# Optimization experiments

Measured on AMD Instinct MI355X. Metric: run time of the kernel, lower is better.

## Reference

```python
import jax, jax.numpy as jnp
import numpy as np


def setup_inputs() -> dict:
    key = jax.random.key(0)
    kq, kk, kv = jax.random.split(key, 3)
    B, H, S, D = 2, 16, 2048, 64
    Q = jax.random.normal(kq, (B, H, S, D), dtype=jnp.float32)
    K = jax.random.normal(kk, (B, H, S, D), dtype=jnp.float32)
    V = jax.random.normal(kv, (B, H, S, D), dtype=jnp.float32)
    # causal mask: 1 = keep, 0 = masked (masked_fill on mask == 0)
    mask = jnp.tril(jnp.ones((S, S), dtype=bool))[None, None, :, :]
    return {"V": V, "Q": Q, "K": K, "Fk": D, "mask": mask}


def reference(V, Q, K, Fk, mask):
    scale = 1.0 / jnp.sqrt(jnp.asarray(Fk, dtype=jnp.float32))
    # [B,H,S,S] scores
    C = jnp.einsum("bhqd,bhkd->bhqk", Q, K) * scale
    C = jnp.where(mask, C, jnp.asarray(-1e9, dtype=C.dtype))
    C = jax.nn.softmax(C, axis=-1)
    return jnp.einsum("bhqk,bhkd->bhqd", C, V)
```

## Files before the change

kernel.cpp:

```cpp
#include <hip/hip_runtime.h>
#include <hip/hip_bf16.h>

typedef __bf16 bf16x8 __attribute__((ext_vector_type(8)));
typedef __bf16 bf16x4 __attribute__((ext_vector_type(4)));
typedef __bf16 bf16x2 __attribute__((ext_vector_type(2)));
typedef float f32x4 __attribute__((ext_vector_type(4)));
typedef float f32x16 __attribute__((ext_vector_type(16)));

#define S_LEN 2048
#define D_DIM 64
#define NQT   32

static __device__ __forceinline__ unsigned pk2(float a, float b) {
  bf16x2 t; t[0] = (__bf16)a; t[1] = (__bf16)b;
  return __builtin_bit_cast(unsigned, t);
}

__global__ __launch_bounds__(256) void preprocess_kernel(
    const float* __restrict__ Kg, const float* __restrict__ Vg,
    unsigned char* __restrict__ Kb, unsigned char* __restrict__ Vt) {
  __shared__ float buf[2048];
  const int tid  = threadIdx.x;
  const int tile = blockIdx.x;
  const float* kg = Kg + (long)tile * 2048;
  const float* vg = Vg + (long)tile * 2048;
  unsigned char* kb = Kb + (long)tile * 4096;
  unsigned char* vt = Vt + (long)tile * 4096;

  const int l = tid & 63, f = tid >> 6, h = l >> 5;

  {
    const float* kr = kg + (l & 31) * 64 + f * 16 + h * 8;
    float4 a = *reinterpret_cast<const float4*>(kr);
    float4 b = *reinterpret_cast<const float4*>(kr + 4);
    bf16x8 t;
    t[0]=(__bf16)a.x; t[1]=(__bf16)a.y; t[2]=(__bf16)a.z; t[3]=(__bf16)a.w;
    t[4]=(__bf16)b.x; t[5]=(__bf16)b.y; t[6]=(__bf16)b.z; t[7]=(__bf16)b.w;
    *reinterpret_cast<bf16x8*>(kb + tid * 16) = t;
  }
  #pragma unroll
  for (int i = 0; i < 2; ++i) {
    int idx = tid + 256 * i;
    *reinterpret_cast<float4*>(buf + idx * 4) =
        *reinterpret_cast<const float4*>(vg + idx * 4);
  }
  __syncthreads();
  {
    int dt = f >> 1, ks = f & 1;
    int d  = dt * 32 + (l & 31);
    int k0 = ks * 16 + h * 8;
    bf16x8 t;
    #pragma unroll
    for (int j = 0; j < 8; ++j) t[j] = (__bf16)buf[(k0 + j) * 64 + d];
    *reinterpret_cast<bf16x8*>(vt + tid * 16) = t;
  }
}

__global__ __launch_bounds__(256, 4) void attn_fwd_pair(
    const float* __restrict__ Qg, const unsigned char* __restrict__ Kb,
    const unsigned char* __restrict__ Vt, float* __restrict__ Og) {
  __shared__ float o_sm[4][32][68];
  __shared__ float m_sm[4][32];
  __shared__ float l_sm[4][32];

  const int tid  = threadIdx.x;
  const int lane = tid & 63;
  const int w    = tid >> 6;
  const int qc   = lane & 31;
  const int h    = lane >> 5;

  const int lb = blockIdx.x;
  const int e  = lb & 7;
  const int s  = lb >> 3;
  const int bh = e + 8 * (s >> 5);
  const int pi = s & 31;
  const long base = (long)bh * (S_LEN * D_DIM);

  const unsigned char* kb_bh = Kb + (long)bh * 64 * 4096 + lane * 16;
  const unsigned char* vt_bh = Vt + (long)bh * 64 * 4096 + lane * 16;

  bf16x8 kfr[4], vfr[4];
  auto ldK = [&](int kt) {
    const unsigned char* p = kb_bh + (long)kt * 4096;
    #pragma unroll
    for (int t = 0; t < 4; ++t)
      kfr[t] = *reinterpret_cast<const bf16x8*>(p + t * 1024);
  };
  auto ldV = [&](int kt) {
    const unsigned char* p = vt_bh + (long)kt * 4096;
    #pragma unroll
    for (int t = 0; t < 4; ++t)
      vfr[t] = *reinterpret_cast<const bf16x8*>(p + t * 1024);
  };

  #pragma unroll
  for (int phase = 0; phase < 2; ++phase) {
    const int qg = phase ? pi : (63 - pi);
    const int q0 = qg * 32;
    const int NT = qg + 1;

    bf16x8 qf[4];
    {
      const float qsc = 0.125f * 1.44269504f;
      const float* qp = Qg + base + (long)(q0 + qc) * D_DIM + h * 8;
      #pragma unroll
      for (int t = 0; t < 4; ++t) {
        float4 f0 = *reinterpret_cast<const float4*>(qp + t * 16);
        float4 f1 = *reinterpret_cast<const float4*>(qp + t * 16 + 4);
        bf16x8 q;
        q[0]=(__bf16)(f0.x*qsc); q[1]=(__bf16)(f0.y*qsc);
        q[2]=(__bf16)(f0.z*qsc); q[3]=(__bf16)(f0.w*qsc);
        q[4]=(__bf16)(f1.x*qsc); q[5]=(__bf16)(f1.y*qsc);
        q[6]=(__bf16)(f1.z*qsc); q[7]=(__bf16)(f1.w*qsc);
        qf[t] = q;
      }
    }

    f32x16 po0, po1;
    #pragma unroll
    for (int r = 0; r < 16; ++r) { po0[r] = 0.f; po1[r] = 0.f; }
    float m_run = -1e30f, l_run = 0.f;

    ldK(w);
    ldV(w);

    for (int kt = w; kt < NT; kt += 4) {
      const bool more = (kt + 4 < NT);

      f32x16 sa;
      #pragma unroll
      for (int r = 0; r < 16; ++r) sa[r] = 0.f;
      __builtin_amdgcn_s_setprio(1);
      #pragma unroll
      for (int t = 0; t < 4; ++t)
        sa = __builtin_amdgcn_mfma_f32_32x32x16_bf16(kfr[t], qf[t], sa, 0, 0, 0);
      __builtin_amdgcn_s_setprio(0);

      if (more) ldK(kt + 4);

      if (kt == NT - 1) {
        #pragma unroll
        for (int r = 0; r < 16; ++r)
          if (((r & 3) + 8 * (r >> 2) + 4 * h) > qc) sa[r] = -1e30f;
      }

      float rmax;
      {
        float a0 = fmaxf(fmaxf(sa[0], sa[1]),  fmaxf(sa[2], sa[3]));
        float a1 = fmaxf(fmaxf(sa[4], sa[5]),  fmaxf(sa[6], sa[7]));
        float a2 = fmaxf(fmaxf(sa[8], sa[9]),  fmaxf(sa[10], sa[11]));
        float a3 = fmaxf(fmaxf(sa[12], sa[13]), fmaxf(sa[14], sa[15]));
        rmax = fmaxf(fmaxf(a0, a1), fmaxf(a2, a3));
        rmax = fmaxf(rmax, __shfl_xor(rmax, 32));
      }

      if (__any(rmax > m_run + 8.0f)) {
        float mn    = fmaxf(m_run, rmax);
        float alpha = exp2f(m_run - mn);
        m_run = mn;
        l_run *= alpha;
        #pragma unroll
        for (int r = 0; r < 16; ++r) {
          float ar = __shfl(alpha, (r & 3) + 8 * (r >> 2) + 4 * h);
          po0[r] *= ar;
          po1[r] *= ar;
        }
      }

      #pragma unroll
      for (int r = 0; r < 16; ++r) sa[r] = exp2f(sa[r] - m_run);
      {
        float s0 = (sa[0] + sa[1]) + (sa[2] + sa[3]);
        float s1 = (sa[4] + sa[5]) + (sa[6] + sa[7]);
        float s2 = (sa[8] + sa[9]) + (sa[10] + sa[11]);
        float s3 = (sa[12] + sa[13]) + (sa[14] + sa[15]);
        float rs = (s0 + s1) + (s2 + s3);
        l_run += rs + __shfl_xor(rs, 32);
      }

      bf16x8 pa0, pa1;
      {
        unsigned k0 = pk2(sa[0], sa[1]),   k1 = pk2(sa[2], sa[3]);
        unsigned k2 = pk2(sa[4], sa[5]),   k3 = pk2(sa[6], sa[7]);
        unsigned k4 = pk2(sa[8], sa[9]),   k5 = pk2(sa[10], sa[11]);
        unsigned k6 = pk2(sa[12], sa[13]), k7 = pk2(sa[14], sa[15]);
        unsigned x02 = h ? k0 : k2, x13 = h ? k1 : k3;
        unsigned x46 = h ? k4 : k6, x57 = h ? k5 : k7;
        unsigned p02 = (unsigned)__shfl_xor((int)x02, 32);
        unsigned p13 = (unsigned)__shfl_xor((int)x13, 32);
        unsigned p46 = (unsigned)__shfl_xor((int)x46, 32);
        unsigned p57 = (unsigned)__shfl_xor((int)x57, 32);
        union { unsigned u[4]; bf16x8 v; } a, b;
        a.u[0] = h ? p02 : k0;  a.u[1] = h ? p13 : k1;
        a.u[2] = h ? k2 : p02;  a.u[3] = h ? k3 : p13;
        b.u[0] = h ? p46 : k4;  b.u[1] = h ? p57 : k5;
        b.u[2] = h ? k6 : p46;  b.u[3] = h ? k7 : p57;
        pa0 = a.v;
        pa1 = b.v;
      }

      __builtin_amdgcn_s_setprio(1);
      po0 = __builtin_amdgcn_mfma_f32_32x32x16_bf16(pa0, vfr[0], po0, 0, 0, 0);
      po0 = __builtin_amdgcn_mfma_f32_32x32x16_bf16(pa1, vfr[1], po0, 0, 0, 0);
      po1 = __builtin_amdgcn_mfma_f32_32x32x16_bf16(pa0, vfr[2], po1, 0, 0, 0);
      po1 = __builtin_amdgcn_mfma_f32_32x32x16_bf16(pa1, vfr[3], po1, 0, 0, 0);
      __builtin_amdgcn_s_setprio(0);

      if (more) ldV(kt + 4);
    }

    if (phase) __syncthreads();
    #pragma unroll
    for (int r = 0; r < 16; ++r) {
      int crow = (r & 3) + 8 * (r >> 2) + 4 * h;
      o_sm[w][crow][qc]      = po0[r];
      o_sm[w][crow][qc + 32] = po1[r];
    }
    if (h == 0) { m_sm[w][qc] = m_run; l_sm[w][qc] = l_run; }
    __syncthreads();

    {
      const int q  = tid >> 3;
      const int d0 = (tid & 7) * 8;
      float m0 = m_sm[0][q], m1 = m_sm[1][q];
      float m2 = m_sm[2][q], m3 = m_sm[3][q];
      float M  = fmaxf(fmaxf(m0, m1), fmaxf(m2, m3));
      float a0 = exp2f(m0 - M), a1 = exp2f(m1 - M);
      float a2 = exp2f(m2 - M), a3 = exp2f(m3 - M);
      float inv = 1.0f / (a0 * l_sm[0][q] + a1 * l_sm[1][q]
                        + a2 * l_sm[2][q] + a3 * l_sm[3][q]);
      float* og = Og + base + (long)(q0 + q) * D_DIM + d0;
      #pragma unroll
      for (int half = 0; half < 2; ++half) {
        float4 x0 = *reinterpret_cast<const float4*>(&o_sm[0][q][d0 + 4 * half]);
        float4 x1 = *reinterpret_cast<const float4*>(&o_sm[1][q][d0 + 4 * half]);
        float4 x2 = *reinterpret_cast<const float4*>(&o_sm[2][q][d0 + 4 * half]);
        float4 x3 = *reinterpret_cast<const float4*>(&o_sm[3][q][d0 + 4 * half]);
        float4 o;
        o.x = (a0 * x0.x + a1 * x1.x + a2 * x2.x + a3 * x3.x) * inv;
        o.y = (a0 * x0.y + a1 * x1.y + a2 * x2.y + a3 * x3.y) * inv;
        o.z = (a0 * x0.z + a1 * x1.z + a2 * x2.z + a3 * x3.z) * inv;
        o.w = (a0 * x0.w + a1 * x1.w + a2 * x2.w + a3 * x3.w) * inv;
        *reinterpret_cast<float4*>(og + 4 * half) = o;
      }
    }
  }
}

__global__ __launch_bounds__(256) void attn_fwd_fallback(
    const float* __restrict__ Vg, const float* __restrict__ Qg,
    const float* __restrict__ Kg, float* __restrict__ Og) {
  __shared__ __align__(16) unsigned char k_lds[64 * 128];
  __shared__ __align__(16) unsigned char vt_lds[64 * 128];
  __shared__ __align__(16) unsigned char p_lds[4][16 * 128];

  const int tid  = threadIdx.x;
  const int lane = tid & 63;
  const int w    = tid >> 6;
  const int lr   = lane & 15;
  const int lg   = lane >> 4;
  const int swz  = (lr & 7) << 4;

  const int lb = blockIdx.x;
  const int e  = lb & 7;
  const int s  = lb >> 3;
  const int bh = e + 8 * (s >> 5);
  const int qs = s & 31;
  const int qt = (qs & 1) ? (NQT - 1 - (qs >> 1)) : (qs >> 1);
  const long base = (long)bh * (S_LEN * D_DIM);
  const int q0 = qt * 64;

  bf16x8 qf[2];
  {
    const float qsc = 0.125f * 1.44269504f;
    const float* qp = Qg + base + (q0 + w * 16 + lr) * D_DIM + lg * 8;
    #pragma unroll
    for (int c = 0; c < 2; ++c) {
      float4 f0 = *reinterpret_cast<const float4*>(qp + c * 32);
      float4 f1 = *reinterpret_cast<const float4*>(qp + c * 32 + 4);
      bf16x8 t;
      t[0]=(__bf16)(f0.x*qsc); t[1]=(__bf16)(f0.y*qsc);
      t[2]=(__bf16)(f0.z*qsc); t[3]=(__bf16)(f0.w*qsc);
      t[4]=(__bf16)(f1.x*qsc); t[5]=(__bf16)(f1.y*qsc);
      t[6]=(__bf16)(f1.z*qsc); t[7]=(__bf16)(f1.w*qsc);
      qf[c] = t;
    }
  }
  bf16x8 onesf;
  #pragma unroll
  for (int j = 0; j < 8; ++j) onesf[j] = (lr == 0) ? (__bf16)1.0f : (__bf16)0.0f;

  f32x4 po[4], pl;
  float m_run = -1e30f;
  #pragma unroll
  for (int j = 0; j < 4; ++j) po[j] = (f32x4){0.f,0.f,0.f,0.f};
  pl = (f32x4){0.f,0.f,0.f,0.f};

  float4 kreg[4];
  float  vreg[16];
  const int d_ = lane;
  const int kb = w;

  auto load_regs = [&](int kt) {
    const float* kg = Kg + base + kt * (64 * D_DIM);
    #pragma unroll
    for (int i = 0; i < 4; ++i) {
      int idx = tid + 256 * i;
      int r = idx >> 4, f4 = idx & 15;
      kreg[i] = *reinterpret_cast<const float4*>(kg + r * 64 + f4 * 4);
    }
    const float* vg = Vg + base + kt * (64 * D_DIM);
    #pragma unroll
    for (int j = 0; j < 8; ++j) {
      vreg[j]     = vg[(kb * 8 + j) * 64 + d_];
      vreg[8 + j] = vg[((kb + 4) * 8 + j) * 64 + d_];
    }
  };
  auto write_buf = [&]() {
    #pragma unroll
    for (int i = 0; i < 4; ++i) {
      int idx = tid + 256 * i;
      int r = idx >> 4, f4 = idx & 15;
      bf16x4 t;
      t[0]=(__bf16)kreg[i].x; t[1]=(__bf16)kreg[i].y;
      t[2]=(__bf16)kreg[i].z; t[3]=(__bf16)kreg[i].w;
      int b = r * 128 + ((f4 * 8) ^ ((r & 7) << 4));
      *reinterpret_cast<bf16x4*>(&k_lds[b]) = t;
    }
    bf16x8 t0, t1;
    #pragma unroll
    for (int j = 0; j < 8; ++j) { t0[j] = (__bf16)vreg[j]; t1[j] = (__bf16)vreg[8+j]; }
    int b0 = d_ * 128 + ((kb * 16) ^ ((d_ & 7) << 4));
    int b1 = d_ * 128 + (((kb + 4) * 16) ^ ((d_ & 7) << 4));
    *reinterpret_cast<bf16x8*>(&vt_lds[b0]) = t0;
    *reinterpret_cast<bf16x8*>(&vt_lds[b1]) = t1;
  };

  load_regs(0);
  write_buf();
  __syncthreads();

  for (int kt = 0; kt <= qt; ++kt) {
    const bool last = (kt == qt);
    if (!last) load_regs(kt + 1);

    f32x4 sa[4];
    #pragma unroll
    for (int ct = 0; ct < 4; ++ct) sa[ct] = (f32x4){0.f,0.f,0.f,0.f};
    #pragma unroll
    for (int ct = 0; ct < 4; ++ct) {
      #pragma unroll
      for (int c = 0; c < 2; ++c) {
        int b = (ct * 16 + lr) * 128 + ((lg * 16 + c * 64) ^ swz);
        bf16x8 kf = *reinterpret_cast<const bf16x8*>(&k_lds[b]);
        sa[ct] = __builtin_amdgcn_mfma_f32_16x16x32_bf16(kf, qf[c], sa[ct], 0, 0, 0);
      }
    }
    if (last) {
      #pragma unroll
      for (int ct = 0; ct < 4; ++ct)
        #pragma unroll
        for (int j = 0; j < 4; ++j)
          if (ct * 16 + lg * 4 + j > w * 16 + lr) sa[ct][j] = -1e30f;
    }
    float rmax = sa[0][0];
    #pragma unroll
    for (int ct = 0; ct < 4; ++ct)
      #pragma unroll
      for (int j = 0; j < 4; ++j) rmax = fmaxf(rmax, sa[ct][j]);
    rmax = fmaxf(rmax, __shfl_xor(rmax, 16));
    rmax = fmaxf(rmax, __shfl_xor(rmax, 32));
    float mn    = fmaxf(m_run, rmax);
    float alpha = exp2f(m_run - mn);
    m_run = mn;
    #pragma unroll
    for (int ct = 0; ct < 4; ++ct) {
      bf16x4 t;
      #pragma unroll
      for (int j = 0; j < 4; ++j) t[j] = (__bf16)exp2f(sa[ct][j] - mn);
      int b = lr * 128 + ((ct * 32 + lg * 8) ^ swz);
      *reinterpret_cast<bf16x4*>(&p_lds[w][b]) = t;
    }
    float aj[4];
    #pragma unroll
    for (int j = 0; j < 4; ++j) aj[j] = __shfl(alpha, (lane & 48) | (lg * 4 + j));
    #pragma unroll
    for (int j = 0; j < 4; ++j) {
      pl[j] *= aj[j];
      #pragma unroll
      for (int dt = 0; dt < 4; ++dt) po[dt][j] *= aj[j];
    }
    #pragma unroll
    for (int c = 0; c < 2; ++c) {
      int ab = lr * 128 + ((lg * 16 + c * 64) ^ swz);
      bf16x8 pa = *reinterpret_cast<const bf16x8*>(&p_lds[w][ab]);
      pl = __builtin_amdgcn_mfma_f32_16x16x32_bf16(pa, onesf, pl, 0, 0, 0);
      #pragma unroll
      for (int dt = 0; dt < 4; ++dt) {
        int vb_ = (dt * 16 + lr) * 128 + ((lg * 16 + c * 64) ^ swz);
        bf16x8 vb = *reinterpret_cast<const bf16x8*>(&vt_lds[vb_]);
        po[dt] = __builtin_amdgcn_mfma_f32_16x16x32_bf16(pa, vb, po[dt], 0, 0, 0);
      }
    }
    if (!last) {
      __syncthreads();
      write_buf();
      __syncthreads();
    }
  }
  #pragma unroll
  for (int j = 0; j < 4; ++j) {
    float lv  = __shfl(pl[j], lane & 48);
    float inv = 1.0f / lv;
    int row = q0 + w * 16 + lg * 4 + j;
    #pragma unroll
    for (int dt = 0; dt < 4; ++dt)
      Og[base + row * D_DIM + dt * 16 + lr] = po[dt][j] * inv;
  }
}

extern "C" void kernel_launch(void* const* d_in, const int* in_sizes, int n_in,
                              void* d_out, int out_size, void* d_ws, size_t ws_size,
                              hipStream_t stream) {
  const float* V = (const float*)d_in[0];
  const float* Q = (const float*)d_in[1];
  const float* K = (const float*)d_in[2];
  float* O = (float*)d_out;
  const size_t need = (size_t)2 * 32 * 64 * 4096;
  if (ws_size >= need) {
    unsigned char* Kb = (unsigned char*)d_ws;
    unsigned char* Vt = Kb + (size_t)32 * 64 * 4096;
    preprocess_kernel<<<dim3(2048), dim3(256), 0, stream>>>(K, V, Kb, Vt);
    attn_fwd_pair<<<dim3(1024), dim3(256), 0, stream>>>(Q, Kb, Vt, O);
  } else {
    attn_fwd_fallback<<<dim3(1024), dim3(256), 0, stream>>>(V, Q, K, O);
  }
}
```

Baseline: 61.91 us.

## Process two 32-row query tiles per workgroup to reuse K/V fragments

Each workgroup now handles a 64-row query block as two 32-row sub-tiles that share every loaded K and V fragment, halving K/V global traffic per query. The grid shrinks from 1024 to 512 blocks and the launch bound drops to 2 waves per SIMD to make room for the doubled accumulators. The causal diagonal is handled by skipping sub-tile A on the last key tile and masking each sub-tile on its own diagonal tile. The risks are lower occupancy, less latency hiding, and fewer blocks to balance the causal work across CUs.

```diff
diff --git a/kernel.cpp b/kernel.cpp
--- a/kernel.cpp
+++ b/kernel.cpp
@@ -56,7 +56,7 @@
   }
 }
 
-__global__ __launch_bounds__(256, 4) void attn_fwd_pair(
+__global__ __launch_bounds__(256, 2) void attn_fwd_q64(
     const float* __restrict__ Qg, const unsigned char* __restrict__ Kb,
     const unsigned char* __restrict__ Vt, float* __restrict__ Og) {
   __shared__ float o_sm[4][32][68];
@@ -69,11 +69,11 @@
   const int qc   = lane & 31;
   const int h    = lane >> 5;
 
-  const int lb = blockIdx.x;
-  const int e  = lb & 7;
-  const int s  = lb >> 3;
-  const int bh = e + 8 * (s >> 5);
-  const int pi = s & 31;
+  const int b  = blockIdx.x;
+  const int e  = b & 7;
+  const int s  = b >> 3;
+  const int bh = e + 8 * (s >> 4);
+  const int pi = s & 15;
   const long base = (long)bh * (S_LEN * D_DIM);
 
   const unsigned char* kb_bh = Kb + (long)bh * 64 * 4096 + lane * 16;
@@ -93,123 +93,69 @@
       vfr[t] = *reinterpret_cast<const bf16x8*>(p + t * 1024);
   };
 
-  #pragma unroll
-  for (int phase = 0; phase < 2; ++phase) {
-    const int qg = phase ? pi : (63 - pi);
-    const int q0 = qg * 32;
-    const int NT = qg + 1;
-
-    bf16x8 qf[4];
+  auto process = [&](f32x16& sa, float& m_run, float& l_run,
+                     f32x16& po0, f32x16& po1) {
+    float rmax;
     {
-      const float qsc = 0.125f * 1.44269504f;
-      const float* qp = Qg + base + (long)(q0 + qc) * D_DIM + h * 8;
-      #pragma unroll
-      for (int t = 0; t < 4; ++t) {
-        float4 f0 = *reinterpret_cast<const float4*>(qp + t * 16);
-        float4 f1 = *reinterpret_cast<const float4*>(qp + t * 16 + 4);
-        bf16x8 q;
-        q[0]=(__bf16)(f0.x*qsc); q[1]=(__bf16)(f0.y*qsc);
-        q[2]=(__bf16)(f0.z*qsc); q[3]=(__bf16)(f0.w*qsc);
-        q[4]=(__bf16)(f1.x*qsc); q[5]=(__bf16)(f1.y*qsc);
-        q[6]=(__bf16)(f1.z*qsc); q[7]=(__bf16)(f1.w*qsc);
-        qf[t] = q;
-      }
-    }
-
-    f32x16 po0, po1;
-    #pragma unroll
-    for (int r = 0; r < 16; ++r) { po0[r] = 0.f; po1[r] = 0.f; }
-    float m_run = -1e30f, l_run = 0.f;
-
-    ldK(w);
-    ldV(w);
-
-    for (int kt = w; kt < NT; kt += 4) {
-      const bool more = (kt + 4 < NT);
-
-      f32x16 sa;
-      #pragma unroll
-      for (int r = 0; r < 16; ++r) sa[r] = 0.f;
-      __builtin_amdgcn_s_setprio(1);
-      #pragma unroll
-      for (int t = 0; t < 4; ++t)
-        sa = __builtin_amdgcn_mfma_f32_32x32x16_bf16(kfr[t], qf[t], sa, 0, 0, 0);
-      __builtin_amdgcn_s_setprio(0);
-
-      if (more) ldK(kt + 4);
-
-      if (kt == NT - 1) {
-        #pragma unroll
-        for (int r = 0; r < 16; ++r)
-          if (((r & 3) + 8 * (r >> 2) + 4 * h) > qc) sa[r] = -1e30f;
-      }
-
-      float rmax;
-      {
-        float a0 = fmaxf(fmaxf(sa[0], sa[1]),  fmaxf(sa[2], sa[3]));
-        float a1 = fmaxf(fmaxf(sa[4], sa[5]),  fmaxf(sa[6], sa[7]));
-        float a2 = fmaxf(fmaxf(sa[8], sa[9]),  fmaxf(sa[10], sa[11]));
-        float a3 = fmaxf(fmaxf(sa[12], sa[13]), fmaxf(sa[14], sa[15]));
-        rmax = fmaxf(fmaxf(a0, a1), fmaxf(a2, a3));
-        rmax = fmaxf(rmax, __shfl_xor(rmax, 32));
-      }
-
-      if (__any(rmax > m_run + 8.0f)) {
-        float mn    = fmaxf(m_run, rmax);
-        float alpha = exp2f(m_run - mn);
-        m_run = mn;
-        l_run *= alpha;
-        #pragma unroll
-        for (int r = 0; r < 16; ++r) {
-          float ar = __shfl(alpha, (r & 3) + 8 * (r >> 2) + 4 * h);
-          po0[r] *= ar;
-          po1[r] *= ar;
-        }
-      }
-
-      #pragma unroll
-      for (int r = 0; r < 16; ++r) sa[r] = exp2f(sa[r] - m_run);
-      {
-        float s0 = (sa[0] + sa[1]) + (sa[2] + sa[3]);
-        float s1 = (sa[4] + sa[5]) + (sa[6] + sa[7]);
-        float s2 = (sa[8] + sa[9]) + (sa[10] + sa[11]);
-        float s3 = (sa[12] + sa[13]) + (sa[14] + sa[15]);
-        float rs = (s0 + s1) + (s2 + s3);
-        l_run += rs + __shfl_xor(rs, 32);
-      }
-
-      bf16x8 pa0, pa1;
-      {
-        unsigned k0 = pk2(sa[0], sa[1]),   k1 = pk2(sa[2], sa[3]);
-        unsigned k2 = pk2(sa[4], sa[5]),   k3 = pk2(sa[6], sa[7]);
-        unsigned k4 = pk2(sa[8], sa[9]),   k5 = pk2(sa[10], sa[11]);
-        unsigned k6 = pk2(sa[12], sa[13]), k7 = pk2(sa[14], sa[15]);
-        unsigned x02 = h ? k0 : k2, x13 = h ? k1 : k3;
-        unsigned x46 = h ? k4 : k6, x57 = h ? k5 : k7;
-        unsigned p02 = (unsigned)__shfl_xor((int)x02, 32);
-        unsigned p13 = (unsigned)__shfl_xor((int)x13, 32);
-        unsigned p46 = (unsigned)__shfl_xor((int)x46, 32);
-        unsigned p57 = (unsigned)__shfl_xor((int)x57, 32);
-        union { unsigned u[4]; bf16x8 v; } a, b;
-        a.u[0] = h ? p02 : k0;  a.u[1] = h ? p13 : k1;
-        a.u[2] = h ? k2 : p02;  a.u[3] = h ? k3 : p13;
-        b.u[0] = h ? p46 : k4;  b.u[1] = h ? p57 : k5;
-        b.u[2] = h ? k6 : p46;  b.u[3] = h ? k7 : p57;
-        pa0 = a.v;
-        pa1 = b.v;
-      }
-
-      __builtin_amdgcn_s_setprio(1);
-      po0 = __builtin_amdgcn_mfma_f32_32x32x16_bf16(pa0, vfr[0], po0, 0, 0, 0);
-      po0 = __builtin_amdgcn_mfma_f32_32x32x16_bf16(pa1, vfr[1], po0, 0, 0, 0);
-      po1 = __builtin_amdgcn_mfma_f32_32x32x16_bf16(pa0, vfr[2], po1, 0, 0, 0);
-      po1 = __builtin_amdgcn_mfma_f32_32x32x16_bf16(pa1, vfr[3], po1, 0, 0, 0);
-      __builtin_amdgcn_s_setprio(0);
-
-      if (more) ldV(kt + 4);
-    }
-
-    if (phase) __syncthreads();
+      float a0 = fmaxf(fmaxf(sa[0], sa[1]),  fmaxf(sa[2], sa[3]));
+      float a1 = fmaxf(fmaxf(sa[4], sa[5]),  fmaxf(sa[6], sa[7]));
+      float a2 = fmaxf(fmaxf(sa[8], sa[9]),  fmaxf(sa[10], sa[11]));
+      float a3 = fmaxf(fmaxf(sa[12], sa[13]), fmaxf(sa[14], sa[15]));
+      rmax = fmaxf(fmaxf(a0, a1), fmaxf(a2, a3));
+      rmax = fmaxf(rmax, __shfl_xor(rmax, 32));
+    }
+    if (__any(rmax > m_run + 8.0f)) {
+      float mn    = fmaxf(m_run, rmax);
+      float alpha = exp2f(m_run - mn);
+      m_run = mn;
+      l_run *= alpha;
+      #pragma unroll
+      for (int r = 0; r < 16; ++r) {
+        float ar = __shfl(alpha, (r & 3) + 8 * (r >> 2) + 4 * h);
+        po0[r] *= ar;
+        po1[r] *= ar;
+      }
+    }
+    #pragma unroll
+    for (int r = 0; r < 16; ++r) sa[r] = exp2f(sa[r] - m_run);
+    {
+      float s0 = (sa[0] + sa[1]) + (sa[2] + sa[3]);
+      float s1 = (sa[4] + sa[5]) + (sa[6] + sa[7]);
+      float s2 = (sa[8] + sa[9]) + (sa[10] + sa[11]);
+      float s3 = (sa[12] + sa[13]) + (sa[14] + sa[15]);
+      float rs = (s0 + s1) + (s2 + s3);
+      l_run += rs + __shfl_xor(rs, 32);
+    }
+    bf16x8 pa0, pa1;
+    {
+      unsigned k0 = pk2(sa[0], sa[1]),   k1 = pk2(sa[2], sa[3]);
+      unsigned k2 = pk2(sa[4], sa[5]),   k3 = pk2(sa[6], sa[7]);
+      unsigned k4 = pk2(sa[8], sa[9]),   k5 = pk2(sa[10], sa[11]);
+      unsigned k6 = pk2(sa[12], sa[13]), k7 = pk2(sa[14], sa[15]);
+      unsigned x02 = h ? k0 : k2, x13 = h ? k1 : k3;
+      unsigned x46 = h ? k4 : k6, x57 = h ? k5 : k7;
+      unsigned p02 = (unsigned)__shfl_xor((int)x02, 32);
+      unsigned p13 = (unsigned)__shfl_xor((int)x13, 32);
+      unsigned p46 = (unsigned)__shfl_xor((int)x46, 32);
+      unsigned p57 = (unsigned)__shfl_xor((int)x57, 32);
+      union { unsigned u[4]; bf16x8 v; } a2, b2;
+      a2.u[0] = h ? p02 : k0;  a2.u[1] = h ? p13 : k1;
+      a2.u[2] = h ? k2 : p02;  a2.u[3] = h ? k3 : p13;
+      b2.u[0] = h ? p46 : k4;  b2.u[1] = h ? p57 : k5;
+      b2.u[2] = h ? k6 : p46;  b2.u[3] = h ? k7 : p57;
+      pa0 = a2.v;
+      pa1 = b2.v;
+    }
+    __builtin_amdgcn_s_setprio(1);
+    po0 = __builtin_amdgcn_mfma_f32_32x32x16_bf16(pa0, vfr[0], po0, 0, 0, 0);
+    po0 = __builtin_amdgcn_mfma_f32_32x32x16_bf16(pa1, vfr[1], po0, 0, 0, 0);
+    po1 = __builtin_amdgcn_mfma_f32_32x32x16_bf16(pa0, vfr[2], po1, 0, 0, 0);
+    po1 = __builtin_amdgcn_mfma_f32_32x32x16_bf16(pa1, vfr[3], po1, 0, 0, 0);
+    __builtin_amdgcn_s_setprio(0);
+  };
+
+  auto submerge = [&](const f32x16& po0, const f32x16& po1,
+                      float m_run, float l_run, int qbase) {
     #pragma unroll
     for (int r = 0; r < 16; ++r) {
       int crow = (r & 3) + 8 * (r >> 2) + 4 * h;
@@ -218,7 +164,6 @@
     }
     if (h == 0) { m_sm[w][qc] = m_run; l_sm[w][qc] = l_run; }
     __syncthreads();
-
     {
       const int q  = tid >> 3;
       const int d0 = (tid & 7) * 8;
@@ -229,7 +174,7 @@
       float a2 = exp2f(m2 - M), a3 = exp2f(m3 - M);
       float inv = 1.0f / (a0 * l_sm[0][q] + a1 * l_sm[1][q]
                         + a2 * l_sm[2][q] + a3 * l_sm[3][q]);
-      float* og = Og + base + (long)(q0 + q) * D_DIM + d0;
+      float* og = Og + base + (long)(qbase + q) * D_DIM + d0;
       #pragma unroll
       for (int half = 0; half < 2; ++half) {
         float4 x0 = *reinterpret_cast<const float4*>(&o_sm[0][q][d0 + 4 * half]);
@@ -244,6 +189,89 @@
         *reinterpret_cast<float4*>(og + 4 * half) = o;
       }
     }
+  };
+
+  for (int phase = 0; phase < 2; ++phase) {
+    const int g  = phase ? pi : (31 - pi);
+    const int q0 = g * 64;
+    const int NT = 2 * g + 2;
+
+    bf16x8 qfA[4], qfB[4];
+    {
+      const float qsc = 0.125f * 1.44269504f;
+      const float* qpA = Qg + base + (long)(q0 + qc) * D_DIM + h * 8;
+      const float* qpB = qpA + 32 * D_DIM;
+      #pragma unroll
+      for (int t = 0; t < 4; ++t) {
+        float4 f0 = *reinterpret_cast<const float4*>(qpA + t * 16);
+        float4 f1 = *reinterpret_cast<const float4*>(qpA + t * 16 + 4);
+        bf16x8 q;
+        q[0]=(__bf16)(f0.x*qsc); q[1]=(__bf16)(f0.y*qsc);
+        q[2]=(__bf16)(f0.z*qsc); q[3]=(__bf16)(f0.w*qsc);
+        q[4]=(__bf16)(f1.x*qsc); q[5]=(__bf16)(f1.y*qsc);
+        q[6]=(__bf16)(f1.z*qsc); q[7]=(__bf16)(f1.w*qsc);
+        qfA[t] = q;
+        f0 = *reinterpret_cast<const float4*>(qpB + t * 16);
+        f1 = *reinterpret_cast<const float4*>(qpB + t * 16 + 4);
+        q[0]=(__bf16)(f0.x*qsc); q[1]=(__bf16)(f0.y*qsc);
+        q[2]=(__bf16)(f0.z*qsc); q[3]=(__bf16)(f0.w*qsc);
+        q[4]=(__bf16)(f1.x*qsc); q[5]=(__bf16)(f1.y*qsc);
+        q[6]=(__bf16)(f1.z*qsc); q[7]=(__bf16)(f1.w*qsc);
+        qfB[t] = q;
+      }
+    }
+
+    f32x16 poA0, poA1, poB0, poB1;
+    #pragma unroll
+    for (int r = 0; r < 16; ++r) { poA0[r]=0.f; poA1[r]=0.f; poB0[r]=0.f; poB1[r]=0.f; }
+    float mA = -1e30f, lA = 0.f, mB = -1e30f, lB = 0.f;
+
+    ldK(w);
+    ldV(w);
+
+    for (int kt = w; kt < NT; kt += 4) {
+      const bool more = (kt + 4 < NT);
+      const bool doA  = (kt != NT - 1);
+
+      f32x16 saA, saB;
+      __builtin_amdgcn_s_setprio(1);
+      if (doA) {
+        #pragma unroll
+        for (int r = 0; r < 16; ++r) saA[r] = 0.f;
+        #pragma unroll
+        for (int t = 0; t < 4; ++t)
+          saA = __builtin_amdgcn_mfma_f32_32x32x16_bf16(kfr[t], qfA[t], saA, 0, 0, 0);
+      }
+      #pragma unroll
+      for (int r = 0; r < 16; ++r) saB[r] = 0.f;
+      #pragma unroll
+      for (int t = 0; t < 4; ++t)
+        saB = __builtin_amdgcn_mfma_f32_32x32x16_bf16(kfr[t], qfB[t], saB, 0, 0, 0);
+      __builtin_amdgcn_s_setprio(0);
+
+      if (more) ldK(kt + 4);
+
+      if (kt == NT - 2) {
+        #pragma unroll
+        for (int r = 0; r < 16; ++r)
+          if (((r & 3) + 8 * (r >> 2) + 4 * h) > qc) saA[r] = -1e30f;
+      }
+      if (kt == NT - 1) {
+        #pragma unroll
+        for (int r = 0; r < 16; ++r)
+          if (((r & 3) + 8 * (r >> 2) + 4 * h) > qc) saB[r] = -1e30f;
+      }
+
+      if (doA) process(saA, mA, lA, poA0, poA1);
+      process(saB, mB, lB, poB0, poB1);
+
+      if (more) ldV(kt + 4);
+    }
+
+    if (phase) __syncthreads();
+    submerge(poA0, poA1, mA, lA, q0);
+    __syncthreads();
+    submerge(poB0, poB1, mB, lB, q0 + 32);
   }
 }
 
@@ -431,7 +459,7 @@
     unsigned char* Kb = (unsigned char*)d_ws;
     unsigned char* Vt = Kb + (size_t)32 * 64 * 4096;
     preprocess_kernel<<<dim3(2048), dim3(256), 0, stream>>>(K, V, Kb, Vt);
-    attn_fwd_pair<<<dim3(1024), dim3(256), 0, stream>>>(Q, Kb, Vt, O);
+    attn_fwd_q64<<<dim3(512), dim3(256), 0, stream>>>(Q, Kb, Vt, O);
   } else {
     attn_fwd_fallback<<<dim3(1024), dim3(256), 0, stream>>>(V, Q, K, O);
   }
```

Measured after the change: 58.05 us, median of 3. 1.07x faster.
